# Performance work log

Hardware: AMD Instinct MI355X
Metric: run time of the kernel (lower is better)

## Reference

```python
import jax, jax.numpy as jnp
import numpy as np

N_NODES = 100000
N_EDGES = 3200000
DIMS = [32, 256, 1024, 1024, 256, 6]


def setup_inputs() -> dict:
    key = jax.random.key(0)
    ks = jax.random.split(key, 2 + 2 * 5)
    inp = {
        "x": jax.random.normal(ks[0], (N_NODES, DIMS[0]), dtype=jnp.float32),
        "edge_index": jax.random.randint(ks[1], (2, N_EDGES), 0, N_NODES, dtype=jnp.int64),
    }
    for i in range(5):
        fan_in, fan_out = DIMS[i], DIMS[i + 1]
        scale = (2.0 / (fan_in + fan_out)) ** 0.5  # glorot-ish
        inp[f"W{i+1}"] = jax.random.normal(ks[2 + 2 * i], (fan_in, fan_out), dtype=jnp.float32) * scale
        inp[f"b{i+1}"] = jnp.zeros((fan_out,), dtype=jnp.float32)
    return inp


def _gcn_forward(x, edge_index, Ws, bs):
    N = x.shape[0]
    # add self loops (PyG GCNConv default)
    loop = jnp.arange(N, dtype=edge_index.dtype)
    src = jnp.concatenate([edge_index[0], loop])
    dst = jnp.concatenate([edge_index[1], loop])
    # symmetric normalization: deg computed on target index (gcn_norm)
    deg = jax.ops.segment_sum(jnp.ones_like(dst, dtype=x.dtype), dst, num_segments=N)
    dinv = jnp.where(deg > 0, jax.lax.rsqrt(deg), 0.0)
    norm = (dinv[src] * dinv[dst])[:, None]  # [E+N, 1]

    def conv(h, W, b):
        h = h @ W                                    # dense linear
        msg = h[src] * norm                          # gather + scale
        agg = jax.ops.segment_sum(msg, dst, num_segments=N)  # scatter-add
        return agg + b

    h = x
    for i in range(4):
        h = jax.nn.relu(conv(h, Ws[i], bs[i]))
    return conv(h, Ws[4], bs[4])


def reference(x, edge_index, W1, b1, W2, b2, W3, b3, W4, b4, W5, b5):
    return _gcn_forward(x, edge_index, (W1, W2, W3, W4, W5), (b1, b2, b3, b4, b5))
```

## Files before the change

kernel.cpp:

```cpp
#include <hip/hip_runtime.h>

typedef unsigned char u8;
typedef unsigned short u16;
typedef unsigned int u32;
typedef __bf16 bf16_t;
typedef bf16_t bf16x8 __attribute__((ext_vector_type(8)));
typedef float f32x4 __attribute__((ext_vector_type(4)));
typedef float f32x2 __attribute__((ext_vector_type(2)));

#define LDS_PTR(p) ((__attribute__((address_space(3))) unsigned int*)(p))
#define GLB_PTR(p) ((const __attribute__((address_space(1))) unsigned int*)(p))

#define BSH 9
#define BCAP 32768

static __device__ __forceinline__ float bf2f(u16 h) {
  u32 u = ((u32)h) << 16;
  return __builtin_bit_cast(float, u);
}
static __device__ __forceinline__ u16 f2bf(float f) {
  u32 u = __builtin_bit_cast(u32, f);
  u += 0x7fffu + ((u >> 16) & 1u);
  return (u16)(u >> 16);
}

__global__ void detect_kernel(const int* __restrict__ ei, const u16* __restrict__ x,
                              int* __restrict__ flags, int* __restrict__ zp, int zn) {
  __shared__ int cnt;
  if (threadIdx.x == 0) cnt = 0;
  __syncthreads();
  if (blockIdx.x == 0) {
    if (ei[1 + 2 * threadIdx.x] != 0) atomicAdd(&cnt, 1);
    __syncthreads();
    if (threadIdx.x == 0) flags[0] = (cnt == 0) ? 1 : 0;
  } else if (blockIdx.x == 1) {
    u32 u = x[threadIdx.x];
    u32 e = (u >> 7) & 0xFF;
    if (e >= 0x60 && e <= 0x83) atomicAdd(&cnt, 1);
    __syncthreads();
    if (threadIdx.x == 0) flags[1] = (cnt >= 240) ? 0 : 1;
  } else {
    for (int i = threadIdx.x; i < zn; i += 256) zp[i] = 0;
  }
}

static __device__ __forceinline__ int eidx(const void* ei, size_t i, int m) {
  return m ? (int)((const long long*)ei)[i] : ((const int*)ei)[i];
}

__global__ void zero_out_kernel(void* __restrict__ out, int n, const int* __restrict__ flags) {
  int i = blockIdx.x * 256 + threadIdx.x;
  if (i < n) {
    if (flags[1]) ((float*)out)[i] = 0.0f;
    else ((u16*)out)[i] = 0;
  }
}

struct CvtArgs {
  const void* src[10];
  u16* dst[10];
  int K[10];
  int N[10];
  int start[11];
};
__global__ void convert_all_kernel(CvtArgs a, const int* __restrict__ flags) {
  int idx = blockIdx.x * 256 + threadIdx.x;
  int f32 = flags[1];
#pragma unroll
  for (int t = 0; t < 10; ++t) {
    if (idx >= a.start[t] && idx < a.start[t + 1]) {
      int local = idx - a.start[t];
      int K = a.K[t], N = a.N[t];
      int k = local / N, n = local - k * N;
      float v = f32 ? ((const float*)a.src[t])[local] : bf2f(((const u16*)a.src[t])[local]);
      a.dst[t][(size_t)n * K + k] = f2bf(v);
    }
  }
}

__global__ __launch_bounds__(256) void bin_kernel(const void* __restrict__ ei,
                                                  int* __restrict__ gcur,
                                                  int2* __restrict__ pairs, int E, int Nn,
                                                  const int* __restrict__ flags, int nblk) {
  __shared__ int h[256];
  __shared__ int base[256];
  const int m = flags[0];
  const int nb = (Nn + (1 << BSH) - 1) >> BSH;
  const int per = (E + nblk - 1) / nblk;
  const int e0 = blockIdx.x * per;
  const int e1 = (e0 + per < E) ? e0 + per : E;
  for (int i = threadIdx.x; i < nb; i += 256) h[i] = 0;
  __syncthreads();
  for (int e = e0 + threadIdx.x; e < e1; e += 256) {
    int d = eidx(ei, (size_t)E + e, m);
    if ((u32)d < (u32)Nn) atomicAdd(&h[d >> BSH], 1);
  }
  __syncthreads();
  for (int i = threadIdx.x; i < nb; i += 256) {
    base[i] = atomicAdd(&gcur[i], h[i]);
    h[i] = 0;
  }
  __syncthreads();
  for (int e = e0 + threadIdx.x; e < e1; e += 256) {
    int d = eidx(ei, (size_t)E + e, m);
    if ((u32)d >= (u32)Nn) continue;
    int s = eidx(ei, (size_t)e, m);
    if ((u32)s >= (u32)Nn) s = 0;
    int b = d >> BSH;
    int p = base[b] + atomicAdd(&h[b], 1);
    if (p < BCAP) pairs[(size_t)b * BCAP + p] = make_int2(s, d);
  }
}

__global__ __launch_bounds__(256) void bucket_scan_kernel(const int* __restrict__ gcur,
                                                          int* __restrict__ gbase, int NB) {
  __shared__ int sd[256];
  int tid = threadIdx.x;
  int v = (tid < NB) ? gcur[tid] : 0;
  if (v > BCAP) v = BCAP;
  sd[tid] = v;
  __syncthreads();
  for (int s = 1; s < 256; s <<= 1) {
    int t = (tid >= s) ? sd[tid - s] : 0;
    __syncthreads();
    sd[tid] += t;
    __syncthreads();
  }
  if (tid < NB) gbase[tid] = sd[tid] - v;
}

__global__ __launch_bounds__(512) void bucket_finalize_kernel(
    const int2* __restrict__ pairs, const int* __restrict__ gcur,
    const int* __restrict__ gbase, int* __restrict__ rowp, float* __restrict__ dinv,
    int* __restrict__ csr, int Nn) {
  __shared__ int cnt[512];
  __shared__ int scn[512];
  const int b = blockIdx.x;
  const int n0 = b << BSH;
  const int tid = threadIdx.x;
  cnt[tid] = 0;
  __syncthreads();
  int tot = gcur[b];
  if (tot > BCAP) tot = BCAP;
  for (int i = tid; i < tot; i += 512) {
    int2 pr = pairs[(size_t)b * BCAP + i];
    atomicAdd(&cnt[pr.y - n0], 1);
  }
  __syncthreads();
  int myc = cnt[tid];
  scn[tid] = myc;
  __syncthreads();
  for (int s = 1; s < 512; s <<= 1) {
    int t = (tid >= s) ? scn[tid - s] : 0;
    __syncthreads();
    scn[tid] += t;
    __syncthreads();
  }
  const int node = n0 + tid;
  const int start = gbase[b] + scn[tid] - myc;
  if (node < Nn) {
    rowp[node] = start;
    dinv[node] = rsqrtf((float)(myc + 1));
    if (node == Nn - 1) rowp[Nn] = gbase[b] + scn[tid];
  }
  cnt[tid] = start;
  __syncthreads();
  for (int i = tid; i < tot; i += 512) {
    int2 pr = pairs[(size_t)b * BCAP + i];
    int p = atomicAdd(&cnt[pr.y - n0], 1);
    csr[p] = pr.x;
  }
}

template <int NPW, int ACT, bool SRCF, bool DSTF>
__global__ __launch_bounds__(256) void spmm_narrow_kernel(
    const void* __restrict__ Hb, void* __restrict__ Gb,
    const int* __restrict__ rowp, const int* __restrict__ csr,
    const float* __restrict__ dinv, const u16* __restrict__ bias,
    int relu, int Nn, int src_stride, int dst_stride, const int* __restrict__ flags) {
  constexpr int G = 64 / NPW;
  constexpr int B = 16;
  const int lane = threadIdx.x & 63;
  const int col = lane & (G - 1);
  const int node = blockIdx.x * 4 * NPW + (threadIdx.x >> 6) * NPW + (lane / G);
  const bool anode = node < Nn;
  const bool act = anode && (col < ACT);
  int sf32 = 0, of32 = 0;
  if (SRCF) sf32 = flags[1];
  if (DSTF) of32 = flags[1];
  const u16* Hs = (const u16*)Hb;
  const float* Hf = (const float*)Hb;

  int e0 = 0, cnt = 0;
  if (anode) {
    e0 = rowp[node];
    cnt = rowp[node + 1] - e0;
  }
  float acc = 0.0f;
  for (int jb = 0; jb < cnt; jb += B) {
    int s[B];
    float wv[B];
#pragma unroll
    for (int j = 0; j < B; ++j) {
      bool val = (jb + j) < cnt;
      s[j] = val ? csr[e0 + jb + j] : node;
      wv[j] = val ? dinv[s[j]] : 0.0f;
    }
    float v[B];
#pragma unroll
    for (int j = 0; j < B; ++j) {
      size_t idx = (size_t)s[j] * src_stride + col;
      v[j] = act ? ((SRCF && sf32) ? Hf[idx] : bf2f(Hs[idx])) : 0.0f;
    }
#pragma unroll
    for (int j = 0; j < B; ++j) acc += wv[j] * v[j];
  }
  if (!act) return;
  const float wi = dinv[node];
  {
    size_t idx = (size_t)node * src_stride + col;
    acc += wi * ((SRCF && sf32) ? Hf[idx] : bf2f(Hs[idx]));
  }
  float v = acc * wi;
  if (bias) v += bf2f(bias[col]);
  if (relu) v = fmaxf(v, 0.0f);
  size_t didx = (size_t)node * dst_stride + col;
  if (DSTF && of32) ((float*)Gb)[didx] = v;
  else ((u16*)Gb)[didx] = f2bf(v);
}

template <int W>
__global__ __launch_bounds__(256) void spmm_fp8_kernel(
    const u8* __restrict__ Hq, u16* __restrict__ Gout,
    const int* __restrict__ rowp, const int* __restrict__ csr,
    const float* __restrict__ dinv, int n0, int n1, int dst_stride) {
  constexpr int BPL = W / 64;
  constexpr int ND = BPL / 4;
  constexpr int B = (W == 1024) ? 8 : 16;
  const int lane = threadIdx.x & 63;
  const int node = __builtin_amdgcn_readfirstlane(n0 + blockIdx.x * 4 + (threadIdx.x >> 6));
  if (node >= n1) return;
  const int off = lane * BPL;
  f32x2 acc[2 * ND] = {};

  auto dec = [&](const u32* d, float w) {
    f32x2 w2 = {w, w};
#pragma unroll
    for (int q = 0; q < ND; ++q) {
      f32x2 a = __builtin_amdgcn_cvt_pk_f32_fp8((int)d[q], false);
      f32x2 b = __builtin_amdgcn_cvt_pk_f32_fp8((int)d[q], true);
      acc[2 * q] += w2 * a;
      acc[2 * q + 1] += w2 * b;
    }
  };

  const int e1r = rowp[node + 1];
  int e = rowp[node];
  for (; e + B <= e1r; e += B) {
    int s[B];
#pragma unroll
    for (int j = 0; j < B; ++j) s[j] = csr[e + j];
    float wv[B];
#pragma unroll
    for (int j = 0; j < B; ++j) wv[j] = dinv[s[j]];
    u32 v[B][ND];
#pragma unroll
    for (int j = 0; j < B; ++j) {
      const u8* p = Hq + (size_t)s[j] * W + off;
      if constexpr (ND == 4) *(int4*)&v[j][0] = *(const int4*)p;
      else v[j][0] = *(const u32*)p;
    }
#pragma unroll
    for (int j = 0; j < B; ++j) dec(v[j], wv[j]);
  }
  for (; e < e1r; ++e) {
    int s = csr[e];
    u32 v[ND];
    const u8* p = Hq + (size_t)s * W + off;
    if constexpr (ND == 4) *(int4*)&v[0] = *(const int4*)p;
    else v[0] = *(const u32*)p;
    dec(v, dinv[s]);
  }
  const float wi = dinv[node];
  {
    u32 v[ND];
    const u8* p = Hq + (size_t)node * W + off;
    if constexpr (ND == 4) *(int4*)&v[0] = *(const int4*)p;
    else v[0] = *(const u32*)p;
    dec(v, wi);
  }

  u32 d[2 * ND];
#pragma unroll
  for (int k = 0; k < 2 * ND; ++k) {
    float v0 = acc[k].x * wi, v1 = acc[k].y * wi;
    d[k] = (u32)f2bf(v0) | ((u32)f2bf(v1) << 16);
  }
  u16* gp = Gout + (size_t)(node - n0) * dst_stride + off;
  if constexpr (ND == 4) {
    ((int4*)gp)[0] = make_int4((int)d[0], (int)d[1], (int)d[2], (int)d[3]);
    ((int4*)gp)[1] = make_int4((int)d[4], (int)d[5], (int)d[6], (int)d[7]);
  } else {
    *(int2*)gp = make_int2((int)d[0], (int)d[1]);
  }
}

__global__ __launch_bounds__(256) void spmm_u8_kernel(
    const u8* __restrict__ Hq, u16* __restrict__ G,
    const int* __restrict__ rowp, const int* __restrict__ csr,
    const float* __restrict__ dinv, const u32* __restrict__ maxbits,
    const u16* __restrict__ bias, int relu, int Nn, int dst_stride) {
  constexpr int B = 16;
  const int lane = threadIdx.x & 63;
  const int node = __builtin_amdgcn_readfirstlane(blockIdx.x * 4 + (threadIdx.x >> 6));
  if (node >= Nn) return;
  const int off = lane * 4;
  float mx = __builtin_bit_cast(float, *maxbits);
  float sq = mx > 0.0f ? mx * (1.0f / 127.0f) : 0.0f;
  float acc[4] = {};
  float wsum = 0.0f;

  auto dec = [&](u32 d, float w) {
    acc[0] += w * (float)(d & 0xffu);
    acc[1] += w * (float)((d >> 8) & 0xffu);
    acc[2] += w * (float)((d >> 16) & 0xffu);
    acc[3] += w * (float)(d >> 24);
    wsum += w;
  };

  const int e1 = rowp[node + 1];
  int e = rowp[node];
  for (; e + B <= e1; e += B) {
    int s[B];
#pragma unroll
    for (int j = 0; j < B; ++j) s[j] = csr[e + j];
    float wv[B];
#pragma unroll
    for (int j = 0; j < B; ++j) wv[j] = dinv[s[j]];
    u32 v[B];
#pragma unroll
    for (int j = 0; j < B; ++j) v[j] = *(const u32*)(Hq + (size_t)s[j] * 256 + off);
#pragma unroll
    for (int j = 0; j < B; ++j) dec(v[j], wv[j]);
  }
  for (; e < e1; ++e) {
    int s = csr[e];
    dec(*(const u32*)(Hq + (size_t)s * 256 + off), dinv[s]);
  }
  const float wi = dinv[node];
  dec(*(const u32*)(Hq + (size_t)node * 256 + off), wi);

  float vals[4];
#pragma unroll
  for (int k = 0; k < 4; ++k) {
    float v = (acc[k] - 128.0f * wsum) * wi * sq;
    if (bias) v += bf2f(bias[off + k]);
    if (relu) v = fmaxf(v, 0.0f);
    vals[k] = v;
  }
  u32 d0 = (u32)f2bf(vals[0]) | ((u32)f2bf(vals[1]) << 16);
  u32 d1 = (u32)f2bf(vals[2]) | ((u32)f2bf(vals[3]) << 16);
  *(int2*)(G + (size_t)node * dst_stride + off) = make_int2((int)d0, (int)d1);
}

__global__ void quant_kernel(const u16* __restrict__ t4, u8* __restrict__ t4q,
                             const u32* __restrict__ maxbits, int n4) {
  int i = blockIdx.x * 256 + threadIdx.x;
  if (i >= n4) return;
  float mx = __builtin_bit_cast(float, *maxbits);
  float inv = mx > 0.0f ? 127.0f / mx : 0.0f;
  int2 v = ((const int2*)t4)[i];
  float f0 = bf2f((u16)(v.x & 0xffff)), f1 = bf2f((u16)((u32)v.x >> 16));
  float f2 = bf2f((u16)(v.y & 0xffff)), f3 = bf2f((u16)((u32)v.y >> 16));
  int q0 = (int)rintf(f0 * inv), q1 = (int)rintf(f1 * inv);
  int q2 = (int)rintf(f2 * inv), q3 = (int)rintf(f3 * inv);
  q0 = min(127, max(-127, q0)) + 128; q1 = min(127, max(-127, q1)) + 128;
  q2 = min(127, max(-127, q2)) + 128; q3 = min(127, max(-127, q3)) + 128;
  ((u32*)t4q)[i] = (u32)q0 | ((u32)q1 << 8) | ((u32)q2 << 16) | ((u32)q3 << 24);
}

__global__ __launch_bounds__(256) void gemm_fast_kernel(
    const u16* __restrict__ A, int lda, const u16* __restrict__ Bt,
    u16* __restrict__ C, int ldc, const u16* __restrict__ bias,
    int M, int N, int K, int relu, int fp8out, u32* __restrict__ maxout) {
  __shared__ __align__(16) u16 sA[128 * 64];
  __shared__ __align__(16) u16 sB[128 * 64];
  const int tid = threadIdx.x;
  const int lane = tid & 63;
  const int wave = __builtin_amdgcn_readfirstlane(tid >> 6);
  const int m0 = blockIdx.y * 128, n0 = blockIdx.x * 128;
  const int wm = (wave & 1) * 64, wn = (wave >> 1) * 64;
  const int lr = lane & 15, lq = lane >> 4;
  const int lrow = lane >> 3;
  const int lcol = (lane & 7) * 8;
  f32x4 acc[4][4] = {};

  for (int kb = 0; kb < K; kb += 64) {
#pragma unroll
    for (int it = 0; it < 4; ++it) {
      const int rbase = (it * 4 + wave) * 8;
      int gm = m0 + rbase + lrow;
      if (gm >= M) gm = M - 1;
      __builtin_amdgcn_global_load_lds(GLB_PTR(A + (size_t)gm * lda + kb + lcol),
                                       LDS_PTR(sA + rbase * 64), 16, 0, 0);
      const int gn = n0 + rbase + lrow;
      __builtin_amdgcn_global_load_lds(GLB_PTR(Bt + (size_t)gn * K + kb + lcol),
                                       LDS_PTR(sB + rbase * 64), 16, 0, 0);
    }
    __syncthreads();
#pragma unroll
    for (int ks = 0; ks < 2; ++ks) {
      bf16x8 af[4], bfr[4];
#pragma unroll
      for (int i = 0; i < 4; ++i)
        af[i] = *(const bf16x8*)(sA + (wm + i * 16 + lr) * 64 + ks * 32 + lq * 8);
#pragma unroll
      for (int i = 0; i < 4; ++i)
        bfr[i] = *(const bf16x8*)(sB + (wn + i * 16 + lr) * 64 + ks * 32 + lq * 8);
#pragma unroll
      for (int im = 0; im < 4; ++im)
#pragma unroll
        for (int in = 0; in < 4; ++in)
          acc[im][in] = __builtin_amdgcn_mfma_f32_16x16x32_bf16(af[im], bfr[in], acc[im][in], 0, 0, 0);
    }
    __syncthreads();
  }
  u32 mymax = 0;
#pragma unroll
  for (int im = 0; im < 4; ++im) {
#pragma unroll
    for (int in = 0; in < 4; ++in) {
      int col = n0 + wn + in * 16 + lr;
      float bv = bias ? bf2f(bias[col]) : 0.0f;
#pragma unroll
      for (int r = 0; r < 4; ++r) {
        int row = m0 + wm + im * 16 + lq * 4 + r;
        if (row < M) {
          float v = acc[im][in][r] + bv;
          if (relu) v = fmaxf(v, 0.0f);
          if (maxout) {
            u32 ab = __builtin_bit_cast(u32, v) & 0x7fffffffu;
            mymax = mymax > ab ? mymax : ab;
          }
          if (fp8out) {
            int pk = __builtin_amdgcn_cvt_pk_fp8_f32(v, v, 0, false);
            ((u8*)C)[(size_t)row * ldc + col] = (u8)(pk & 0xff);
          } else {
            C[(size_t)row * ldc + col] = f2bf(v);
          }
        }
      }
    }
  }
  if (maxout) {
    u32* red = (u32*)sA;
    red[tid] = mymax;
    __syncthreads();
    for (int s = 128; s > 0; s >>= 1) {
      if (tid < s) red[tid] = red[tid] > red[tid + s] ? red[tid] : red[tid + s];
      __syncthreads();
    }
    if (tid == 0) atomicMax(maxout, red[0]);
  }
}

#define LP 72
__global__ __launch_bounds__(256) void gemm_small_kernel(
    const u16* __restrict__ A, int lda, const u16* __restrict__ Bt,
    u16* __restrict__ C, int ldc, const u16* __restrict__ bias,
    int M, int N, int K, int relu, int fp8out) {
  __shared__ __align__(16) u16 sA[128 * LP];
  __shared__ __align__(16) u16 sB[128 * LP];
  const int tid = threadIdx.x;
  const int lane = tid & 63, wave = tid >> 6;
  const int m0 = blockIdx.y * 128, n0 = blockIdx.x * 128;
  const int wm = (wave & 1) * 64, wn = (wave >> 1) * 64;
  const int lr = lane & 15;
  const int lq = lane >> 4;
  f32x4 acc[4][4] = {};

  for (int kb = 0; kb < K; kb += 64) {
#pragma unroll
    for (int it = 0; it < 4; ++it) {
      int linear = it * 2048 + tid * 8;
      int row = linear >> 6, kc = linear & 63;
      int gm = m0 + row, gk = kb + kc;
      int4 v = make_int4(0, 0, 0, 0);
      if (gm < M && gk < K) v = *(const int4*)(A + (size_t)gm * lda + gk);
      *(int4*)(sA + row * LP + kc) = v;
    }
#pragma unroll
    for (int it = 0; it < 4; ++it) {
      int linear = it * 2048 + tid * 8;
      int row = linear >> 6, kc = linear & 63;
      int gn = n0 + row, gk = kb + kc;
      int4 v = make_int4(0, 0, 0, 0);
      if (gn < N && gk < K) v = *(const int4*)(Bt + (size_t)gn * K + gk);
      *(int4*)(sB + row * LP + kc) = v;
    }
    __syncthreads();
#pragma unroll
    for (int ks = 0; ks < 2; ++ks) {
      bf16x8 af[4], bfr[4];
#pragma unroll
      for (int i = 0; i < 4; ++i)
        af[i] = *(const bf16x8*)(sA + (wm + i * 16 + lr) * LP + ks * 32 + lq * 8);
#pragma unroll
      for (int i = 0; i < 4; ++i)
        bfr[i] = *(const bf16x8*)(sB + (wn + i * 16 + lr) * LP + ks * 32 + lq * 8);
#pragma unroll
      for (int im = 0; im < 4; ++im)
#pragma unroll
        for (int in = 0; in < 4; ++in)
          acc[im][in] = __builtin_amdgcn_mfma_f32_16x16x32_bf16(af[im], bfr[in], acc[im][in], 0, 0, 0);
    }
    __syncthreads();
  }
#pragma unroll
  for (int im = 0; im < 4; ++im) {
#pragma unroll
    for (int in = 0; in < 4; ++in) {
      int col = n0 + wn + in * 16 + lr;
      if (col >= N) continue;
      float bv = bias ? bf2f(bias[col]) : 0.0f;
#pragma unroll
      for (int r = 0; r < 4; ++r) {
        int row = m0 + wm + im * 16 + lq * 4 + r;
        if (row < M) {
          float v = acc[im][in][r] + bv;
          if (relu) v = fmaxf(v, 0.0f);
          if (fp8out) {
            int pk = __builtin_amdgcn_cvt_pk_fp8_f32(v, v, 0, false);
            ((u8*)C)[(size_t)row * ldc + col] = (u8)(pk & 0xff);
          } else {
            C[(size_t)row * ldc + col] = f2bf(v);
          }
        }
      }
    }
  }
}

extern "C" void kernel_launch(void* const* d_in, const int* in_sizes, int n_in,
                              void* d_out, int out_size, void* d_ws, size_t ws_size,
                              hipStream_t stream) {
  const u16* x  = (const u16*)d_in[0];
  const int* ei = (const int*)d_in[1];

  const int Nn = in_sizes[0] / 32;
  const int E  = in_sizes[1] / 2;
  const int CH = (Nn + 7) / 8;
  const int NR = (Nn + CH - 1) / CH;
  const int NB = (Nn + (1 << BSH) - 1) >> BSH;

  char* w = (char*)d_ws;
  size_t off = 0;
  auto alloc = [&](size_t bytes) -> void* {
    void* p = w + off;
    off = (off + bytes + 255) & ~(size_t)255;
    return p;
  };
  int*   flags  = (int*)alloc(256);
  int*   gcur   = (int*)alloc(1024);
  int*   gbase  = (int*)alloc(1024);
  u32*   tmax   = (u32*)alloc(256);
  int*   rowp   = (int*)alloc((size_t)(Nn + 1) * 4);
  float* dinv   = (float*)alloc((size_t)Nn * 4);
  int*   csr    = (int*)alloc((size_t)E * 4);
  u16*   Wt1    = (u16*)alloc((size_t)32 * 256 * 2);
  u16*   Wt2    = (u16*)alloc((size_t)256 * 1024 * 2);
  u16*   Wt3    = (u16*)alloc((size_t)1024 * 1024 * 2);
  u16*   Wt4    = (u16*)alloc((size_t)1024 * 256 * 2);
  u16*   Wt5    = (u16*)alloc((size_t)256 * 6 * 2);
  u16*   bc1    = (u16*)alloc(256 * 2);
  u16*   bc2    = (u16*)alloc(1024 * 2);
  u16*   bc3    = (u16*)alloc(1024 * 2);
  u16*   bc4    = (u16*)alloc(256 * 2);
  u16*   bc5    = (u16*)alloc(6 * 2);
  size_t selems = (size_t)CH * 1024;
  u16*   S      = (u16*)alloc(selems * 2);
  u16*   H      = (u16*)alloc((size_t)Nn * 1024 * 2);
  const size_t required = off;
  (void)n_in;

  if (ws_size < required) {
    if (ws_size >= 4096) {
      detect_kernel<<<3, 256, 0, stream>>>(ei, x, flags, gcur, 576);
      zero_out_kernel<<<(out_size + 255) / 256, 256, 0, stream>>>(d_out, out_size, flags);
    }
    return;
  }

  u8*  h2q = (u8*)H;
  u8*  t4q = (u8*)H;
  u16* g2  = H + (size_t)Nn * 512;
  u16* t4  = H + (size_t)Nn * 512;
  u8*  h1q = (u8*)(H + (size_t)Nn * 768);
  u16* h3R = H + (size_t)Nn * 768;
  u16* h4  = H + (size_t)Nn * 768;

  int2* pairs = (int2*)H;

  detect_kernel<<<3, 256, 0, stream>>>(ei, x, flags, gcur, 576);
  bin_kernel<<<1024, 256, 0, stream>>>(ei, gcur, pairs, E, Nn, flags, 1024);
  bucket_scan_kernel<<<1, 256, 0, stream>>>(gcur, gbase, NB);
  bucket_finalize_kernel<<<NB, 512, 0, stream>>>(pairs, gcur, gbase, rowp, dinv, csr, Nn);

  {
    CvtArgs a;
    const int Ks[10] = {32, 1, 256, 1, 1024, 1, 1024, 1, 256, 1};
    const int Ns[10] = {256, 256, 1024, 1024, 1024, 1024, 256, 256, 6, 6};
    u16* ds[10] = {Wt1, bc1, Wt2, bc2, Wt3, bc3, Wt4, bc4, Wt5, bc5};
    int cum = 0;
    for (int t = 0; t < 10; ++t) {
      a.src[t] = d_in[2 + t];
      a.dst[t] = ds[t];
      a.K[t] = Ks[t];
      a.N[t] = Ns[t];
      a.start[t] = cum;
      cum += Ks[t] * Ns[t];
    }
    a.start[10] = cum;
    convert_all_kernel<<<(cum + 255) / 256, 256, 0, stream>>>(a, flags);
  }

  const int sg = (Nn + 3) / 4;
  const int mb = (Nn + 127) / 128;

  spmm_narrow_kernel<2, 32, true, false><<<(Nn + 7) / 8, 256, 0, stream>>>(
      x, S, rowp, csr, dinv, nullptr, 0, Nn, 32, 32, flags);
  gemm_small_kernel<<<dim3(2, mb), 256, 0, stream>>>(S, 32, Wt1, (u16*)h1q, 256, bc1,
                                                     Nn, 256, 32, 1, 1);

  spmm_fp8_kernel<256><<<sg, 256, 0, stream>>>(h1q, g2, rowp, csr, dinv, 0, Nn, 256);
  gemm_fast_kernel<<<dim3(8, mb), 256, 0, stream>>>(g2, 256, Wt2, (u16*)h2q, 1024, bc2,
                                                    Nn, 1024, 256, 1, 1, nullptr);

  for (int R = 0; R < NR; ++R) {
    int n0 = R * CH;
    int n1 = n0 + CH < Nn ? n0 + CH : Nn;
    int MR = n1 - n0;
    int mbr = (MR + 127) / 128;
    spmm_fp8_kernel<1024><<<(MR + 3) / 4, 256, 0, stream>>>(h2q, S, rowp, csr, dinv, n0, n1, 1024);
    gemm_fast_kernel<<<dim3(8, mbr), 256, 0, stream>>>(S, 1024, Wt3, h3R, 1024, bc3,
                                                       MR, 1024, 1024, 1, 0, nullptr);
    gemm_fast_kernel<<<dim3(2, mbr), 256, 0, stream>>>(h3R, 1024, Wt4, t4 + (size_t)n0 * 256, 256,
                                                       nullptr, MR, 256, 1024, 0, 0, tmax);
  }

  quant_kernel<<<(Nn * 64 + 255) / 256, 256, 0, stream>>>(t4, t4q, tmax, Nn * 64);

  spmm_u8_kernel<<<sg, 256, 0, stream>>>(t4q, h4, rowp, csr, dinv, tmax, bc4, 1, Nn, 256);

  gemm_small_kernel<<<dim3(1, mb), 256, 0, stream>>>(h4, 256, Wt5, S, 6, nullptr,
                                                     Nn, 6, 256, 0, 0);
  spmm_narrow_kernel<8, 6, false, true><<<(Nn + 31) / 32, 256, 0, stream>>>(
      S, d_out, rowp, csr, dinv, bc5, 0, Nn, 6, 6, flags);
}
```

Measured before the change: 2.097 ms.

## Fold source-side degree scaling into GEMM epilogues and double-buffer SpMM gathers

Moves the per-source dinv factor out of every SpMM inner loop. It is applied once per row in the preceding GEMM epilogue through a rowscale argument, or in a new prescale pass for the input x. This removes the dependent dinv[s] gather per edge and lets the u8 SpMM accumulate raw bytes with packed 16-bit integer adds. The fp8 and u8 SpMM kernels also double-buffer their neighbour-row loads so one batch's loads overlap the previous batch's decode. The risks are that scaling before fp8 quantization changes the rounding, and that the packed u16 sums could overflow on very high-degree nodes.

```diff
diff --git a/kernel.cpp b/kernel.cpp
--- a/kernel.cpp
+++ b/kernel.cpp
@@ -76,6 +76,16 @@
       a.dst[t][(size_t)n * K + k] = f2bf(v);
     }
   }
+}
+
+__global__ void prescale_x_kernel(const void* __restrict__ x, void* __restrict__ xs,
+                                  const float* __restrict__ dinv, int n,
+                                  const int* __restrict__ flags) {
+  int i = blockIdx.x * 256 + threadIdx.x;
+  if (i >= n) return;
+  float w = dinv[i >> 5];
+  if (flags[1]) ((float*)xs)[i] = ((const float*)x)[i] * w;
+  else ((u16*)xs)[i] = f2bf(bf2f(((const u16*)x)[i]) * w);
 }
 
 __global__ __launch_bounds__(256) void bin_kernel(const void* __restrict__ ei,
@@ -199,27 +209,26 @@
   float acc = 0.0f;
   for (int jb = 0; jb < cnt; jb += B) {
     int s[B];
-    float wv[B];
 #pragma unroll
     for (int j = 0; j < B; ++j) {
       bool val = (jb + j) < cnt;
       s[j] = val ? csr[e0 + jb + j] : node;
-      wv[j] = val ? dinv[s[j]] : 0.0f;
     }
     float v[B];
 #pragma unroll
     for (int j = 0; j < B; ++j) {
+      bool val = act && ((jb + j) < cnt);
       size_t idx = (size_t)s[j] * src_stride + col;
-      v[j] = act ? ((SRCF && sf32) ? Hf[idx] : bf2f(Hs[idx])) : 0.0f;
-    }
-#pragma unroll
-    for (int j = 0; j < B; ++j) acc += wv[j] * v[j];
+      v[j] = val ? ((SRCF && sf32) ? Hf[idx] : bf2f(Hs[idx])) : 0.0f;
+    }
+#pragma unroll
+    for (int j = 0; j < B; ++j) acc += v[j];
   }
   if (!act) return;
   const float wi = dinv[node];
   {
     size_t idx = (size_t)node * src_stride + col;
-    acc += wi * ((SRCF && sf32) ? Hf[idx] : bf2f(Hs[idx]));
+    acc += (SRCF && sf32) ? Hf[idx] : bf2f(Hs[idx]);
   }
   float v = acc * wi;
   if (bias) v += bf2f(bias[col]);
@@ -243,58 +252,87 @@
   const int off = lane * BPL;
   f32x2 acc[2 * ND] = {};
 
-  auto dec = [&](const u32* d, float w) {
-    f32x2 w2 = {w, w};
+  auto dec1 = [&](const u32* d) {
 #pragma unroll
     for (int q = 0; q < ND; ++q) {
       f32x2 a = __builtin_amdgcn_cvt_pk_f32_fp8((int)d[q], false);
       f32x2 b = __builtin_amdgcn_cvt_pk_f32_fp8((int)d[q], true);
-      acc[2 * q] += w2 * a;
-      acc[2 * q + 1] += w2 * b;
-    }
-  };
-
-  const int e1r = rowp[node + 1];
-  int e = rowp[node];
-  for (; e + B <= e1r; e += B) {
+      acc[2 * q] += a;
+      acc[2 * q + 1] += b;
+    }
+  };
+  auto ldrow = [&](u32* v, int s) {
+    const u8* p = Hq + (size_t)s * W + off;
+    if constexpr (ND == 4) *(int4*)v = *(const int4*)p;
+    else v[0] = *(const u32*)p;
+  };
+
+  const int e0 = rowp[node];
+  const int cnt = rowp[node + 1] - e0;
+  const int tot = cnt + 1;
+  const int NB2 = (tot + B - 1) / B;
+  const int NBF = NB2 - 1;
+
+  u32 vA[B][ND], vB[B][ND];
+
+  auto ldb_full = [&](u32 (*v)[ND], int k) {
+    const int base = k * B;
     int s[B];
 #pragma unroll
-    for (int j = 0; j < B; ++j) s[j] = csr[e + j];
-    float wv[B];
-#pragma unroll
-    for (int j = 0; j < B; ++j) wv[j] = dinv[s[j]];
-    u32 v[B][ND];
+    for (int j = 0; j < B; ++j) s[j] = csr[e0 + base + j];
+#pragma unroll
+    for (int j = 0; j < B; ++j) ldrow(v[j], s[j]);
+  };
+  auto ldb_last = [&](u32 (*v)[ND]) {
+    const int base = NBF * B;
 #pragma unroll
     for (int j = 0; j < B; ++j) {
-      const u8* p = Hq + (size_t)s[j] * W + off;
-      if constexpr (ND == 4) *(int4*)&v[j][0] = *(const int4*)p;
-      else v[j][0] = *(const u32*)p;
-    }
-#pragma unroll
-    for (int j = 0; j < B; ++j) dec(v[j], wv[j]);
-  }
-  for (; e < e1r; ++e) {
-    int s = csr[e];
-    u32 v[ND];
-    const u8* p = Hq + (size_t)s * W + off;
-    if constexpr (ND == 4) *(int4*)&v[0] = *(const int4*)p;
-    else v[0] = *(const u32*)p;
-    dec(v, dinv[s]);
-  }
+      const int i = base + j;
+      if (i < tot) {
+        int s = (i < cnt) ? csr[e0 + i] : node;
+        ldrow(v[j], s);
+      } else {
+#pragma unroll
+        for (int q = 0; q < ND; ++q) v[j][q] = 0u;
+      }
+    }
+  };
+  auto decfull = [&](u32 (*v)[ND]) {
+#pragma unroll
+    for (int j = 0; j < B; ++j) dec1(v[j]);
+  };
+
+  if (NB2 == 1) {
+    ldb_last(vA);
+    decfull(vA);
+  } else {
+    ldb_last(vA);
+    ldb_full(vB, 0);
+    int k = 1;
+    while (k + 1 < NBF) {
+      decfull(vA);
+      ldb_full(vA, k);
+      decfull(vB);
+      ldb_full(vB, k + 1);
+      k += 2;
+    }
+    if (k < NBF) {
+      decfull(vA);
+      ldb_full(vA, k);
+      decfull(vB);
+      decfull(vA);
+    } else {
+      decfull(vA);
+      decfull(vB);
+    }
+  }
+
   const float wi = dinv[node];
-  {
-    u32 v[ND];
-    const u8* p = Hq + (size_t)node * W + off;
-    if constexpr (ND == 4) *(int4*)&v[0] = *(const int4*)p;
-    else v[0] = *(const u32*)p;
-    dec(v, wi);
-  }
-
   u32 d[2 * ND];
 #pragma unroll
-  for (int k = 0; k < 2 * ND; ++k) {
-    float v0 = acc[k].x * wi, v1 = acc[k].y * wi;
-    d[k] = (u32)f2bf(v0) | ((u32)f2bf(v1) << 16);
+  for (int kk = 0; kk < 2 * ND; ++kk) {
+    float v0 = acc[kk].x * wi, v1 = acc[kk].y * wi;
+    d[kk] = (u32)f2bf(v0) | ((u32)f2bf(v1) << 16);
   }
   u16* gp = Gout + (size_t)(node - n0) * dst_stride + off;
   if constexpr (ND == 4) {
@@ -317,46 +355,86 @@
   const int off = lane * 4;
   float mx = __builtin_bit_cast(float, *maxbits);
   float sq = mx > 0.0f ? mx * (1.0f / 127.0f) : 0.0f;
-  float acc[4] = {};
-  float wsum = 0.0f;
-
-  auto dec = [&](u32 d, float w) {
-    acc[0] += w * (float)(d & 0xffu);
-    acc[1] += w * (float)((d >> 8) & 0xffu);
-    acc[2] += w * (float)((d >> 16) & 0xffu);
-    acc[3] += w * (float)(d >> 24);
-    wsum += w;
-  };
-
-  const int e1 = rowp[node + 1];
-  int e = rowp[node];
-  for (; e + B <= e1; e += B) {
+  u32 aP0 = 0, aP1 = 0;
+
+  auto dec1 = [&](u32 d) {
+    aP0 += d & 0x00ff00ffu;
+    aP1 += (d >> 8) & 0x00ff00ffu;
+  };
+  auto ldrow = [&](u32* v, int s) { *v = *(const u32*)(Hq + (size_t)s * 256 + off); };
+
+  const int e0 = rowp[node];
+  const int cnt = rowp[node + 1] - e0;
+  const int tot = cnt + 1;
+  const int NB2 = (tot + B - 1) / B;
+  const int NBF = NB2 - 1;
+
+  u32 vA[B], vB[B];
+
+  auto ldb_full = [&](u32* v, int k) {
+    const int base = k * B;
     int s[B];
 #pragma unroll
-    for (int j = 0; j < B; ++j) s[j] = csr[e + j];
-    float wv[B];
-#pragma unroll
-    for (int j = 0; j < B; ++j) wv[j] = dinv[s[j]];
-    u32 v[B];
-#pragma unroll
-    for (int j = 0; j < B; ++j) v[j] = *(const u32*)(Hq + (size_t)s[j] * 256 + off);
-#pragma unroll
-    for (int j = 0; j < B; ++j) dec(v[j], wv[j]);
-  }
-  for (; e < e1; ++e) {
-    int s = csr[e];
-    dec(*(const u32*)(Hq + (size_t)s * 256 + off), dinv[s]);
-  }
+    for (int j = 0; j < B; ++j) s[j] = csr[e0 + base + j];
+#pragma unroll
+    for (int j = 0; j < B; ++j) ldrow(&v[j], s[j]);
+  };
+  auto ldb_last = [&](u32* v) {
+    const int base = NBF * B;
+#pragma unroll
+    for (int j = 0; j < B; ++j) {
+      const int i = base + j;
+      if (i < tot) {
+        int s = (i < cnt) ? csr[e0 + i] : node;
+        ldrow(&v[j], s);
+      } else {
+        v[j] = 0u;
+      }
+    }
+  };
+  auto decfull = [&](u32* v) {
+#pragma unroll
+    for (int j = 0; j < B; ++j) dec1(v[j]);
+  };
+
+  if (NB2 == 1) {
+    ldb_last(vA);
+    decfull(vA);
+  } else {
+    ldb_last(vA);
+    ldb_full(vB, 0);
+    int k = 1;
+    while (k + 1 < NBF) {
+      decfull(vA);
+      ldb_full(vA, k);
+      decfull(vB);
+      ldb_full(vB, k + 1);
+      k += 2;
+    }
+    if (k < NBF) {
+      decfull(vA);
+      ldb_full(vA, k);
+      decfull(vB);
+      decfull(vA);
+    } else {
+      decfull(vA);
+      decfull(vB);
+    }
+  }
+
   const float wi = dinv[node];
-  dec(*(const u32*)(Hq + (size_t)node * 256 + off), wi);
-
+  float su[4];
+  su[0] = (float)(aP0 & 0xffffu);
+  su[2] = (float)(aP0 >> 16);
+  su[1] = (float)(aP1 & 0xffffu);
+  su[3] = (float)(aP1 >> 16);
   float vals[4];
 #pragma unroll
-  for (int k = 0; k < 4; ++k) {
-    float v = (acc[k] - 128.0f * wsum) * wi * sq;
-    if (bias) v += bf2f(bias[off + k]);
+  for (int k2 = 0; k2 < 4; ++k2) {
+    float v = (su[k2] - 128.0f * (float)tot) * wi * sq;
+    if (bias) v += bf2f(bias[off + k2]);
     if (relu) v = fmaxf(v, 0.0f);
-    vals[k] = v;
+    vals[k2] = v;
   }
   u32 d0 = (u32)f2bf(vals[0]) | ((u32)f2bf(vals[1]) << 16);
   u32 d1 = (u32)f2bf(vals[2]) | ((u32)f2bf(vals[3]) << 16);
@@ -382,7 +460,8 @@
 __global__ __launch_bounds__(256) void gemm_fast_kernel(
     const u16* __restrict__ A, int lda, const u16* __restrict__ Bt,
     u16* __restrict__ C, int ldc, const u16* __restrict__ bias,
-    int M, int N, int K, int relu, int fp8out, u32* __restrict__ maxout) {
+    int M, int N, int K, int relu, int fp8out, u32* __restrict__ maxout,
+    const float* __restrict__ rowscale) {
   __shared__ __align__(16) u16 sA[128 * 64];
   __shared__ __align__(16) u16 sB[128 * 64];
   const int tid = threadIdx.x;
@@ -438,6 +517,7 @@
         if (row < M) {
           float v = acc[im][in][r] + bv;
           if (relu) v = fmaxf(v, 0.0f);
+          if (rowscale) v *= rowscale[row];
           if (maxout) {
             u32 ab = __builtin_bit_cast(u32, v) & 0x7fffffffu;
             mymax = mymax > ab ? mymax : ab;
@@ -468,7 +548,7 @@
 __global__ __launch_bounds__(256) void gemm_small_kernel(
     const u16* __restrict__ A, int lda, const u16* __restrict__ Bt,
     u16* __restrict__ C, int ldc, const u16* __restrict__ bias,
-    int M, int N, int K, int relu, int fp8out) {
+    int M, int N, int K, int relu, int fp8out, const float* __restrict__ rowscale) {
   __shared__ __align__(16) u16 sA[128 * LP];
   __shared__ __align__(16) u16 sB[128 * LP];
   const int tid = threadIdx.x;
@@ -529,6 +609,7 @@
         if (row < M) {
           float v = acc[im][in][r] + bv;
           if (relu) v = fmaxf(v, 0.0f);
+          if (rowscale) v *= rowscale[row];
           if (fp8out) {
             int pk = __builtin_amdgcn_cvt_pk_fp8_f32(v, v, 0, false);
             ((u8*)C)[(size_t)row * ldc + col] = (u8)(pk & 0xff);
@@ -591,6 +672,7 @@
     return;
   }
 
+  void* xs = (void*)H;
   u8*  h2q = (u8*)H;
   u8*  t4q = (u8*)H;
   u16* g2  = H + (size_t)Nn * 512;
@@ -605,6 +687,8 @@
   bin_kernel<<<1024, 256, 0, stream>>>(ei, gcur, pairs, E, Nn, flags, 1024);
   bucket_scan_kernel<<<1, 256, 0, stream>>>(gcur, gbase, NB);
   bucket_finalize_kernel<<<NB, 512, 0, stream>>>(pairs, gcur, gbase, rowp, dinv, csr, Nn);
+
+  prescale_x_kernel<<<(Nn * 32 + 255) / 256, 256, 0, stream>>>(x, xs, dinv, Nn * 32, flags);
 
   {
     CvtArgs a;
@@ -628,13 +712,13 @@
   const int mb = (Nn + 127) / 128;
 
   spmm_narrow_kernel<2, 32, true, false><<<(Nn + 7) / 8, 256, 0, stream>>>(
-      x, S, rowp, csr, dinv, nullptr, 0, Nn, 32, 32, flags);
+      xs, S, rowp, csr, dinv, nullptr, 0, Nn, 32, 32, flags);
   gemm_small_kernel<<<dim3(2, mb), 256, 0, stream>>>(S, 32, Wt1, (u16*)h1q, 256, bc1,
-                                                     Nn, 256, 32, 1, 1);
+                                                     Nn, 256, 32, 1, 1, dinv);
 
   spmm_fp8_kernel<256><<<sg, 256, 0, stream>>>(h1q, g2, rowp, csr, dinv, 0, Nn, 256);
   gemm_fast_kernel<<<dim3(8, mb), 256, 0, stream>>>(g2, 256, Wt2, (u16*)h2q, 1024, bc2,
-                                                    Nn, 1024, 256, 1, 1, nullptr);
+                                                    Nn, 1024, 256, 1, 1, nullptr, dinv);
 
   for (int R = 0; R < NR; ++R) {
     int n0 = R * CH;
@@ -643,9 +727,10 @@
     int mbr = (MR + 127) / 128;
     spmm_fp8_kernel<1024><<<(MR + 3) / 4, 256, 0, stream>>>(h2q, S, rowp, csr, dinv, n0, n1, 1024);
     gemm_fast_kernel<<<dim3(8, mbr), 256, 0, stream>>>(S, 1024, Wt3, h3R, 1024, bc3,
-                                                       MR, 1024, 1024, 1, 0, nullptr);
+                                                       MR, 1024, 1024, 1, 0, nullptr, nullptr);
     gemm_fast_kernel<<<dim3(2, mbr), 256, 0, stream>>>(h3R, 1024, Wt4, t4 + (size_t)n0 * 256, 256,
-                                                       nullptr, MR, 256, 1024, 0, 0, tmax);
+                                                       nullptr, MR, 256, 1024, 0, 0, tmax,
+                                                       dinv + n0);
   }
 
   quant_kernel<<<(Nn * 64 + 255) / 256, 256, 0, stream>>>(t4, t4q, tmax, Nn * 64);
@@ -653,7 +738,7 @@
   spmm_u8_kernel<<<sg, 256, 0, stream>>>(t4q, h4, rowp, csr, dinv, tmax, bc4, 1, Nn, 256);
 
   gemm_small_kernel<<<dim3(1, mb), 256, 0, stream>>>(h4, 256, Wt5, S, 6, nullptr,
-                                                     Nn, 6, 256, 0, 0);
+                                                     Nn, 6, 256, 0, 0, dinv);
   spmm_narrow_kernel<8, 6, false, true><<<(Nn + 31) / 32, 256, 0, stream>>>(
       S, d_out, rowp, csr, dinv, bc5, 0, Nn, 6, 6, flags);
 }
```

New measurement: 2.114 ms. About the same (+0.8%).
